# Kernel tuning notes

Hardware: AMD Instinct MI355X
Metric: run time of the kernel (lower is better)

## Reference

```python
import jax, jax.numpy as jnp
import numpy as np

B, F, V, E = 4096, 26, 20000, 64
LAYERS = [256, 128, 1]


def setup_inputs() -> dict:
    key = jax.random.key(0)
    ks = jax.random.split(key, 13)
    s = 1.0 / np.sqrt(E)
    inp = {
        "x_idx": jax.random.randint(ks[0], (B, F), 0, V),
        # per-field embedding tables [F, V, E] and linear (bias) tables [F, V, 1]
        "embed_w": jax.random.normal(ks[1], (F, V, E), jnp.float32) * 0.01,
        "embed_b": jax.random.normal(ks[2], (F, V, 1), jnp.float32) * 0.01,
        "attention_w": jax.random.normal(ks[3], (E, E), jnp.float32) * s,
        "attention_b": jax.random.normal(ks[4], (1, E), jnp.float32) * 0.01,
        "attention_p": jax.random.normal(ks[5], (E,), jnp.float32) * 0.01,
        "w0": jax.random.normal(ks[6], (E, LAYERS[0]), jnp.float32) * s,
        "b0": jnp.zeros((LAYERS[0],), jnp.float32),
        "w1": jax.random.normal(ks[7], (LAYERS[0], LAYERS[1]), jnp.float32) * (1.0 / np.sqrt(LAYERS[0])),
        "b1": jnp.zeros((LAYERS[1],), jnp.float32),
        "w2": jax.random.normal(ks[8], (LAYERS[1], LAYERS[2]), jnp.float32) * (1.0 / np.sqrt(LAYERS[1])),
        "b2": jnp.zeros((LAYERS[2],), jnp.float32),
        "bias": jnp.zeros((1,), jnp.float32),
    }
    return inp


def _gather_fields(tables, idx):
    # tables: [F, V, D], idx: [B, F] -> [B, F, D]
    return jax.vmap(lambda tbl, i: tbl[i], in_axes=(0, 1), out_axes=1)(tables, idx)


def reference(x_idx, embed_w, embed_b, attention_w, attention_b, attention_p,
              w0, b0, w1, b1, w2, b2, bias):
    f = embed_w.shape[0]
    xw = _gather_fields(embed_w, x_idx)                      # [B, F, E]
    iu, ju = jnp.triu_indices(f, k=1)                        # P = F*(F-1)/2 pairs, loop order i<j
    pairs = xw[:, iu, :] * xw[:, ju, :]                      # [B, P, E] pairwise FM interactions
    # attention network: relu(pairs @ W + b), score = <p, .>, softmax over pairs
    att_h = jax.nn.relu(jnp.einsum('bpe,ef->bpf', pairs, attention_w) + attention_b)
    scores = jnp.sum(attention_p * att_h, axis=2, keepdims=True)   # [B, P, 1]
    att_out = jax.nn.softmax(scores, axis=1)                       # softmax pooling over pairs
    afm = jnp.sum(att_out * pairs, axis=1)                         # [B, E]
    # MLP head
    h = jax.nn.relu(afm @ w0 + b0)
    h = jax.nn.relu(h @ w1 + b1)
    bilinear = h @ w2 + b2                                         # [B, 1]
    # linear (LR) term from per-field bias tables
    lr = jnp.sum(_gather_fields(embed_b, x_idx), axis=1)           # [B, 1]
    return bilinear + lr + bias
```

## Files before the change

### kernel.cpp

```cpp
#include <hip/hip_runtime.h>
#include <stdint.h>

#define B_N 4096
#define F_N 26
#define V_N 20000
#define E_N 64
#define P_N 325
#define PT  21
#define SPB 8

typedef __attribute__((ext_vector_type(8))) _Float16 half8;
typedef __attribute__((ext_vector_type(4))) _Float16 half4;
typedef __attribute__((ext_vector_type(4))) float floatx4;
typedef __attribute__((ext_vector_type(4))) unsigned int uint4v;

static __device__ __forceinline__ float h2lo(unsigned int v) {
    return (float)__builtin_bit_cast(_Float16, (unsigned short)(v & 0xffffu));
}
static __device__ __forceinline__ float h2hi(unsigned int v) {
    return (float)__builtin_bit_cast(_Float16, (unsigned short)(v >> 16));
}

__global__ __launch_bounds__(512, 4) void anfm_fused_kernel(
    const int* __restrict__ x_idx, const float* __restrict__ embed_w,
    const float* __restrict__ embed_b, const float* __restrict__ att_w,
    const float* __restrict__ att_b, const float* __restrict__ att_p,
    const float* __restrict__ w0, const float* __restrict__ b0,
    const float* __restrict__ w1, const float* __restrict__ b1,
    const float* __restrict__ w2, const float* __restrict__ b2,
    const float* __restrict__ bias, float* __restrict__ out)
{
    __shared__ _Float16 xwb[SPB][F_N][72];
    __shared__ _Float16 WT[64][72];
    __shared__ unsigned short pijL[336];
    __shared__ unsigned int abapL[64];
    __shared__ _Float16 afmL[16][72];
    __shared__ _Float16 h0L[16][264];
    __shared__ float    h1L[16][132];
    __shared__ float    lrL[SPB];

    const int tid  = threadIdx.x;
    const int lane = tid & 63;
    const int wid  = tid >> 6;
    const int c16  = lane & 15;
    const int g    = lane >> 4;
    const int b    = blockIdx.x * SPB + wid;

    int myidx = (lane < F_N) ? x_idx[b * F_N + lane] : 0;
    float lv  = (lane < F_N) ? embed_b[lane * V_N + myidx] : 0.f;
    float4 gv[7];
    #pragma unroll
    for (int it = 0; it < 7; it++) {
        int f = it * 4 + g;
        int fc = (f < F_N) ? f : 0;
        int idxf = __shfl(myidx, fc);
        const float4* src = reinterpret_cast<const float4*>(
            embed_w + ((size_t)(fc * V_N + idxf)) * E_N);
        gv[it] = src[c16];
    }

    if (tid < 336) {
        int p = tid;
        int i = 0, j = 1;
        if (p < P_N) {
            i = (int)((51.0f - sqrtf(2601.0f - 8.0f * (float)p)) * 0.5f);
            if (i * (51 - i) / 2 > p) i--;
            else if ((i + 1) * (50 - i) / 2 <= p) i++;
            j = p - i * (51 - i) / 2 + i + 1;
        }
        pijL[p] = (unsigned short)((i << 8) | j);
    } else if (tid < 400) {
        int n = tid - 336;
        unsigned short abh = __builtin_bit_cast(unsigned short, (_Float16)att_b[n]);
        unsigned short aph = __builtin_bit_cast(unsigned short, (_Float16)att_p[n]);
        abapL[n] = ((unsigned int)aph << 16) | (unsigned int)abh;
    }
    for (int z = tid; z < 576; z += 512) {
        int r = z / 72, c = z - r * 72;
        afmL[8 + r][c] = (_Float16)0.f;
    }
    for (int idx = tid; idx < 64 * 64; idx += 512) {
        int k = idx >> 6, col = idx & 63;
        WT[col][k] = (_Float16)att_w[idx];
    }

    #pragma unroll
    for (int it = 0; it < 7; it++) {
        int f = it * 4 + g;
        if (f < F_N) {
            float4 v = gv[it];
            half4 hv = {(_Float16)v.x, (_Float16)v.y, (_Float16)v.z, (_Float16)v.w};
            *reinterpret_cast<half4*>(&xwb[wid][f][c16 * 4]) = hv;
        }
    }
    __syncthreads();

    half8 bfr[4][2];
    #pragma unroll
    for (int nt = 0; nt < 4; nt++)
        #pragma unroll
        for (int s = 0; s < 2; s++)
            bfr[nt][s] = *reinterpret_cast<const half8*>(
                &WT[nt * 16 + c16][s * 32 + g * 8]);
    uint4v abap[4];
    #pragma unroll
    for (int nt = 0; nt < 4; nt++)
        abap[nt] = *reinterpret_cast<const uint4v*>(&abapL[nt * 16 + g * 4]);

    float acf[16];
    #pragma unroll
    for (int u = 0; u < 16; u++) acf[u] = 0.f;
    float Zp = 0.f;

    #pragma unroll 1
    for (int t = 0; t < PT; t++) {
        int pk = pijL[t * 16 + c16];
        int ri = pk >> 8, rj = pk & 255;
        half8 af[2];
        #pragma unroll
        for (int s = 0; s < 2; s++) {
            half8 xv = *reinterpret_cast<const half8*>(&xwb[wid][ri][s * 32 + g * 8]);
            half8 yv = *reinterpret_cast<const half8*>(&xwb[wid][rj][s * 32 + g * 8]);
            af[s] = xv * yv;
        }
        float scq = 0.f;
        #pragma unroll
        for (int nt = 0; nt < 4; nt++) {
            floatx4 acc = {h2lo(abap[nt][0]), h2lo(abap[nt][1]),
                           h2lo(abap[nt][2]), h2lo(abap[nt][3])};
            acc = __builtin_amdgcn_mfma_f32_16x16x32_f16(bfr[nt][0], af[0], acc, 0, 0, 0);
            acc = __builtin_amdgcn_mfma_f32_16x16x32_f16(bfr[nt][1], af[1], acc, 0, 0, 0);
            #pragma unroll
            for (int r = 0; r < 4; r++)
                scq = fmaf(h2hi(abap[nt][r]), fmaxf(acc[r], 0.f), scq);
        }
        scq += __shfl_xor(scq, 16);
        scq += __shfl_xor(scq, 32);
        float w = (t * 16 + c16 < P_N) ? __expf(scq) : 0.f;
        Zp += w;
        #pragma unroll
        for (int s = 0; s < 2; s++)
            #pragma unroll
            for (int u = 0; u < 8; u++)
                acf[s * 8 + u] = fmaf((float)af[s][u], w, acf[s * 8 + u]);
    }

    #pragma unroll
    for (int msk = 1; msk <= 8; msk <<= 1) {
        Zp += __shfl_xor(Zp, msk);
        #pragma unroll
        for (int u = 0; u < 16; u++) acf[u] += __shfl_xor(acf[u], msk);
    }

    if (c16 == 0) {
        float rZ = 1.f / Zp;
        #pragma unroll
        for (int s = 0; s < 2; s++) {
            half4 o0 = {(_Float16)(acf[s * 8 + 0] * rZ), (_Float16)(acf[s * 8 + 1] * rZ),
                        (_Float16)(acf[s * 8 + 2] * rZ), (_Float16)(acf[s * 8 + 3] * rZ)};
            half4 o1 = {(_Float16)(acf[s * 8 + 4] * rZ), (_Float16)(acf[s * 8 + 5] * rZ),
                        (_Float16)(acf[s * 8 + 6] * rZ), (_Float16)(acf[s * 8 + 7] * rZ)};
            *reinterpret_cast<half4*>(&afmL[wid][s * 32 + g * 8])     = o0;
            *reinterpret_cast<half4*>(&afmL[wid][s * 32 + g * 8 + 4]) = o1;
        }
    }
    #pragma unroll
    for (int off = 32; off; off >>= 1) lv += __shfl_xor(lv, off);
    if (lane == 0) lrL[wid] = lv;
    __syncthreads();


    {
        half8 af0[2];
        #pragma unroll
        for (int s = 0; s < 2; s++)
            af0[s] = *reinterpret_cast<const half8*>(&afmL[c16][s * 32 + g * 8]);
        #pragma unroll
        for (int q = 0; q < 2; q++) {
            int n = (wid * 2 + q) * 16 + c16;
            half8 bf[2];
            #pragma unroll
            for (int s = 0; s < 2; s++)
                #pragma unroll
                for (int u = 0; u < 8; u++)
                    bf[s][u] = (_Float16)w0[(s * 32 + g * 8 + u) * 256 + n];
            floatx4 acc = {0.f, 0.f, 0.f, 0.f};
            acc = __builtin_amdgcn_mfma_f32_16x16x32_f16(af0[0], bf[0], acc, 0, 0, 0);
            acc = __builtin_amdgcn_mfma_f32_16x16x32_f16(af0[1], bf[1], acc, 0, 0, 0);
            float b0n = b0[n];
            #pragma unroll
            for (int r = 0; r < 4; r++)
                h0L[g * 4 + r][n] = (_Float16)fmaxf(acc[r] + b0n, 0.f);
        }
    }
    __syncthreads();

    {
        int n = wid * 16 + c16;
        floatx4 acc = {0.f, 0.f, 0.f, 0.f};
        #pragma unroll
        for (int ks = 0; ks < 8; ks++) {
            half8 af1 = *reinterpret_cast<const half8*>(&h0L[c16][ks * 32 + g * 8]);
            half8 bf;
            #pragma unroll
            for (int u = 0; u < 8; u++)
                bf[u] = (_Float16)w1[(ks * 32 + g * 8 + u) * 128 + n];
            acc = __builtin_amdgcn_mfma_f32_16x16x32_f16(af1, bf, acc, 0, 0, 0);
        }
        float b1n = b1[n];
        #pragma unroll
        for (int r = 0; r < 4; r++)
            h1L[g * 4 + r][n] = fmaxf(acc[r] + b1n, 0.f);
    }
    __syncthreads();

    {
        float part = fmaf(h1L[wid][lane * 2], w2[lane * 2],
                          h1L[wid][lane * 2 + 1] * w2[lane * 2 + 1]);
        #pragma unroll
        for (int off = 32; off; off >>= 1) part += __shfl_xor(part, off);
        if (lane == 0)
            out[blockIdx.x * SPB + wid] = part + b2[0] + bias[0] + lrL[wid];
    }
}

extern "C" void kernel_launch(void* const* d_in, const int* in_sizes, int n_in,
                              void* d_out, int out_size, void* d_ws, size_t ws_size,
                              hipStream_t stream) {
    const int*   x_idx   = (const int*)d_in[0];
    const float* embed_w = (const float*)d_in[1];
    const float* embed_b = (const float*)d_in[2];
    const float* att_w   = (const float*)d_in[3];
    const float* att_b   = (const float*)d_in[4];
    const float* att_p   = (const float*)d_in[5];
    const float* w0      = (const float*)d_in[6];
    const float* b0      = (const float*)d_in[7];
    const float* w1      = (const float*)d_in[8];
    const float* b1      = (const float*)d_in[9];
    const float* w2      = (const float*)d_in[10];
    const float* b2      = (const float*)d_in[11];
    const float* bias    = (const float*)d_in[12];
    float*       out     = (float*)d_out;

    anfm_fused_kernel<<<B_N / SPB, 512, 0, stream>>>(
        x_idx, embed_w, embed_b, att_w, att_b, att_p,
        w0, b0, w1, b1, w2, b2, bias, out);
}
```

Measured before the change: 34.28 us.

## Alias attention and MLP LDS buffers and reload WT fragments per iteration

Overlays the embedding/attention-weight shared buffers with the MLP hidden-activation buffers in one union, shrinking the LDS footprint per block. The attention-weight B fragments are now read from LDS inside the pair loop instead of being held in registers. Launch bounds are raised from 4 to 6 blocks per CU. The aim is higher occupancy from lower LDS and register use, at the cost of extra LDS reads on every loop iteration. With only 512 blocks launched, extra occupancy may buy little.

```diff
diff --git a/kernel.cpp b/kernel.cpp
--- a/kernel.cpp
+++ b/kernel.cpp
@@ -21,7 +21,7 @@
     return (float)__builtin_bit_cast(_Float16, (unsigned short)(v >> 16));
 }
 
-__global__ __launch_bounds__(512, 4) void anfm_fused_kernel(
+__global__ __launch_bounds__(512, 6) void anfm_fused_kernel(
     const int* __restrict__ x_idx, const float* __restrict__ embed_w,
     const float* __restrict__ embed_b, const float* __restrict__ att_w,
     const float* __restrict__ att_b, const float* __restrict__ att_p,
@@ -30,13 +30,19 @@
     const float* __restrict__ w2, const float* __restrict__ b2,
     const float* __restrict__ bias, float* __restrict__ out)
 {
-    __shared__ _Float16 xwb[SPB][F_N][72];
-    __shared__ _Float16 WT[64][72];
+    __shared__ union {
+        struct {
+            _Float16 xwb[SPB][F_N][72];
+            _Float16 WT[64][72];
+        } a;
+        struct {
+            _Float16 h0L[16][264];
+            float    h1L[16][132];
+        } m;
+    } U;
     __shared__ unsigned short pijL[336];
     __shared__ unsigned int abapL[64];
     __shared__ _Float16 afmL[16][72];
-    __shared__ _Float16 h0L[16][264];
-    __shared__ float    h1L[16][132];
     __shared__ float    lrL[SPB];
 
     const int tid  = threadIdx.x;
@@ -81,7 +87,7 @@
     }
     for (int idx = tid; idx < 64 * 64; idx += 512) {
         int k = idx >> 6, col = idx & 63;
-        WT[col][k] = (_Float16)att_w[idx];
+        U.a.WT[col][k] = (_Float16)att_w[idx];
     }
 
     #pragma unroll
@@ -90,18 +96,11 @@
         if (f < F_N) {
             float4 v = gv[it];
             half4 hv = {(_Float16)v.x, (_Float16)v.y, (_Float16)v.z, (_Float16)v.w};
-            *reinterpret_cast<half4*>(&xwb[wid][f][c16 * 4]) = hv;
-        }
-    }
-    __syncthreads();
-
-    half8 bfr[4][2];
-    #pragma unroll
-    for (int nt = 0; nt < 4; nt++)
-        #pragma unroll
-        for (int s = 0; s < 2; s++)
-            bfr[nt][s] = *reinterpret_cast<const half8*>(
-                &WT[nt * 16 + c16][s * 32 + g * 8]);
+            *reinterpret_cast<half4*>(&U.a.xwb[wid][f][c16 * 4]) = hv;
+        }
+    }
+    __syncthreads();
+
     uint4v abap[4];
     #pragma unroll
     for (int nt = 0; nt < 4; nt++)
@@ -119,17 +118,21 @@
         half8 af[2];
         #pragma unroll
         for (int s = 0; s < 2; s++) {
-            half8 xv = *reinterpret_cast<const half8*>(&xwb[wid][ri][s * 32 + g * 8]);
-            half8 yv = *reinterpret_cast<const half8*>(&xwb[wid][rj][s * 32 + g * 8]);
+            half8 xv = *reinterpret_cast<const half8*>(&U.a.xwb[wid][ri][s * 32 + g * 8]);
+            half8 yv = *reinterpret_cast<const half8*>(&U.a.xwb[wid][rj][s * 32 + g * 8]);
             af[s] = xv * yv;
         }
         float scq = 0.f;
         #pragma unroll
         for (int nt = 0; nt < 4; nt++) {
+            half8 bf0 = *reinterpret_cast<const half8*>(
+                &U.a.WT[nt * 16 + c16][g * 8]);
+            half8 bf1 = *reinterpret_cast<const half8*>(
+                &U.a.WT[nt * 16 + c16][32 + g * 8]);
             floatx4 acc = {h2lo(abap[nt][0]), h2lo(abap[nt][1]),
                            h2lo(abap[nt][2]), h2lo(abap[nt][3])};
-            acc = __builtin_amdgcn_mfma_f32_16x16x32_f16(bfr[nt][0], af[0], acc, 0, 0, 0);
-            acc = __builtin_amdgcn_mfma_f32_16x16x32_f16(bfr[nt][1], af[1], acc, 0, 0, 0);
+            acc = __builtin_amdgcn_mfma_f32_16x16x32_f16(bf0, af[0], acc, 0, 0, 0);
+            acc = __builtin_amdgcn_mfma_f32_16x16x32_f16(bf1, af[1], acc, 0, 0, 0);
             #pragma unroll
             for (int r = 0; r < 4; r++)
                 scq = fmaf(h2hi(abap[nt][r]), fmaxf(acc[r], 0.f), scq);
@@ -190,7 +193,7 @@
             float b0n = b0[n];
             #pragma unroll
             for (int r = 0; r < 4; r++)
-                h0L[g * 4 + r][n] = (_Float16)fmaxf(acc[r] + b0n, 0.f);
+                U.m.h0L[g * 4 + r][n] = (_Float16)fmaxf(acc[r] + b0n, 0.f);
         }
     }
     __syncthreads();
@@ -200,7 +203,7 @@
         floatx4 acc = {0.f, 0.f, 0.f, 0.f};
         #pragma unroll
         for (int ks = 0; ks < 8; ks++) {
-            half8 af1 = *reinterpret_cast<const half8*>(&h0L[c16][ks * 32 + g * 8]);
+            half8 af1 = *reinterpret_cast<const half8*>(&U.m.h0L[c16][ks * 32 + g * 8]);
             half8 bf;
             #pragma unroll
             for (int u = 0; u < 8; u++)
@@ -210,13 +213,13 @@
         float b1n = b1[n];
         #pragma unroll
         for (int r = 0; r < 4; r++)
-            h1L[g * 4 + r][n] = fmaxf(acc[r] + b1n, 0.f);
+            U.m.h1L[g * 4 + r][n] = fmaxf(acc[r] + b1n, 0.f);
     }
     __syncthreads();
 
     {
-        float part = fmaf(h1L[wid][lane * 2], w2[lane * 2],
-                          h1L[wid][lane * 2 + 1] * w2[lane * 2 + 1]);
+        float part = fmaf(U.m.h1L[wid][lane * 2], w2[lane * 2],
+                          U.m.h1L[wid][lane * 2 + 1] * w2[lane * 2 + 1]);
         #pragma unroll
         for (int off = 32; off; off >>= 1) part += __shfl_xor(part, off);
         if (lane == 0)
```

Measured after the change: 86.36 us. +151.9%, slower.
